# Optimization experiments

Hardware: AMD Instinct MI355X
Metric: run time of the kernel (lower is better)

Reference implementation:

```python
import jax, jax.numpy as jnp
import numpy as np
from jax import lax

B, C_IN, T = 64, 16, 8192
HID, OUT = 64, 10
NEW_T = T // 4            # two MaxPool1d(2)
N_NODES = B * NEW_T       # 131072
N_EDGES = 2_097_152       # avg degree 16


def setup_inputs() -> dict:
    key = jax.random.key(0)
    ks = jax.random.split(key, 8)
    x = jax.random.normal(ks[0], (B, C_IN, T), dtype=jnp.float32)
    edge_index = jax.random.randint(ks[1], (2, N_EDGES), 0, N_NODES, dtype=jnp.int32)
    s = 0.05
    return {
        "x": x,
        "edge_index": edge_index,
        "conv1_w": jax.random.normal(ks[2], (16, C_IN, 5), dtype=jnp.float32) * s,
        "conv1_b": jnp.zeros((16,), jnp.float32),
        "conv2_w": jax.random.normal(ks[3], (32, 16, 5), dtype=jnp.float32) * s,
        "conv2_b": jnp.zeros((32,), jnp.float32),
        "gcn1_w": jax.random.normal(ks[4], (32, HID), dtype=jnp.float32) * s,
        "gcn1_b": jnp.zeros((HID,), jnp.float32),
        "gcn2_w": jax.random.normal(ks[5], (HID, HID), dtype=jnp.float32) * s,
        "gcn2_b": jnp.zeros((HID,), jnp.float32),
        "cls_w": jax.random.normal(ks[6], (HID, OUT), dtype=jnp.float32) * s,
        "cls_b": jnp.zeros((OUT,), jnp.float32),
    }


def conv1d(x, w, b):
    # x: [B, Cin, T], w: [Cout, Cin, K], padding=2 -> same length
    y = lax.conv_general_dilated(x, w, window_strides=(1,), padding=[(2, 2)],
                                 dimension_numbers=("NCH", "OIH", "NCH"))
    return y + b[None, :, None]


def maxpool2(x):
    # non-overlapping MaxPool1d(kernel=2) over last dim
    b, c, t = x.shape
    return x.reshape(b, c, t // 2, 2).max(axis=-1)


def gcn_conv(x, edge_index, W, b, n):
    # PyG GCNConv: add self-loops, symmetric normalization, scatter-add aggregate
    row, col = edge_index[0], edge_index[1]   # source j, target i
    loop = jnp.arange(n, dtype=row.dtype)
    row = jnp.concatenate([row, loop])
    col = jnp.concatenate([col, loop])
    deg = jax.ops.segment_sum(jnp.ones(row.shape, x.dtype), col, num_segments=n)
    dis = jnp.where(deg > 0, lax.rsqrt(deg), jnp.zeros_like(deg))
    norm = dis[row] * dis[col]                # [E+N]
    xw = x @ W                                # [N, out]
    msg = xw[row] * norm[:, None]             # gather along edges
    out = jax.ops.segment_sum(msg, col, num_segments=n)
    return out + b


def reference(x, edge_index, conv1_w, conv1_b, conv2_w, conv2_b,
              gcn1_w, gcn1_b, gcn2_w, gcn2_b, cls_w, cls_b):
    h = maxpool2(jax.nn.relu(conv1d(x, conv1_w, conv1_b)))     # [B,16,T/2]
    h = maxpool2(jax.nn.relu(conv1d(h, conv2_w, conv2_b)))     # [B,32,T/4]
    feat = h.transpose(0, 2, 1).reshape(-1, 32)                # [B*new_T, 32]
    n = feat.shape[0]
    g = jax.nn.relu(gcn_conv(feat, edge_index, gcn1_w, gcn1_b, n))
    g = jax.nn.relu(gcn_conv(g, edge_index, gcn2_w, gcn2_b, n))
    pooled = g.reshape(B, -1, HID).mean(axis=1)                # [B, HID]
    return pooled @ cls_w + cls_b                               # [B, OUT]
```

## Files before the change

kernel.cpp:

```cpp
#include <hip/hip_runtime.h>
#include <hip/hip_bf16.h>
#include <hip/hip_fp16.h>

#define BATCH 64
#define C_IN 16
#define T0 8192
#define T1 4096
#define T2 2048
#define N_NODES (BATCH * T2)
#define HID 64
#define NOUT 10

#define NCB 256
#define CB_SHIFT 9
#define CB_TGT 512
#define RCAP 9216
#define PC_EDGES 2048
#define PC_CAP 28

#define PK_RMASK 0x1FFFF

#define EC 1024

#define ZROW N_NODES

#define ROWW 24

#define FP8_SCALE 256.0f
#define FP8_SINV  (1.0f / 256.0f)

typedef __fp16 half8 __attribute__((ext_vector_type(8)));
typedef __fp16 half4v __attribute__((ext_vector_type(4)));
typedef float floatx4 __attribute__((ext_vector_type(4)));
typedef float floatx2 __attribute__((ext_vector_type(2)));

__global__ __launch_bounds__(256) void conv1_kernel(const float* __restrict__ x,
    const float* __restrict__ w, const float* __restrict__ bias,
    __fp16* __restrict__ h1) {
  __shared__ __fp16 xs[528 * ROWW];
  int b = blockIdx.x >> 4;
  int tp0 = (blockIdx.x & 15) * 256;
  int t_base = 2 * tp0 - 8;
  const float* xb = x + (size_t)b * C_IN * T0;
  for (int idx = threadIdx.x; idx < 16 * 132; idx += 256) {
    int ci = idx & 15;
    int c4 = idx >> 4;
    int gt = t_base + c4 * 4;
    float4 v = make_float4(0.f, 0.f, 0.f, 0.f);
    if (gt >= 0 && gt + 4 <= T0) v = *(const float4*)(xb + ci * T0 + gt);
    __fp16* d = xs + (c4 * 4) * ROWW + ci;
    d[0] = (__fp16)v.x;
    d[ROWW] = (__fp16)v.y;
    d[2 * ROWW] = (__fp16)v.z;
    d[3 * ROWW] = (__fp16)v.w;
  }
  int ln = threadIdx.x & 15;
  int q = (threadIdx.x & 63) >> 4;
  int wib = threadIdx.x >> 6;
  half8 wb[3];
#pragma unroll
  for (int ks = 0; ks < 3; ++ks) {
    int kk = ks * 2 + (q >> 1);
#pragma unroll
    for (int j = 0; j < 8; ++j) {
      int ci = (q & 1) * 8 + j;
      float wv = (kk < 5) ? w[(ln * 16 + ci) * 5 + kk] : 0.f;
      wb[ks][j] = (__fp16)wv;
    }
  }
  float bv = bias[ln];
  __syncthreads();
  int qh = q >> 1, qo = (q & 1) * 8;
#pragma unroll 2
  for (int mtl = 0; mtl < 8; ++mtl) {
    int mt = wib * 8 + mtl;
    int posb = mt * 16 + ln + qh + 6;
    half8 a0 = *(const half8*)(xs + posb * ROWW + qo);
    half8 a1 = *(const half8*)(xs + (posb + 2) * ROWW + qo);
    half8 a2 = *(const half8*)(xs + (posb + 4) * ROWW + qo);
    floatx4 c0 = {0.f, 0.f, 0.f, 0.f};
    c0 = __builtin_amdgcn_mfma_f32_16x16x32_f16(a0, wb[0], c0, 0, 0, 0);
    c0 = __builtin_amdgcn_mfma_f32_16x16x32_f16(a1, wb[1], c0, 0, 0, 0);
    c0 = __builtin_amdgcn_mfma_f32_16x16x32_f16(a2, wb[2], c0, 0, 0, 0);
    int tp = tp0 + mt * 8 + q * 2;
    size_t o = ((size_t)b * T1 + tp) * 16 + ln;
    h1[o] = (__fp16)fmaxf(fmaxf(c0[0], c0[1]) + bv, 0.f);
    h1[o + 16] = (__fp16)fmaxf(fmaxf(c0[2], c0[3]) + bv, 0.f);
  }
}

__global__ __launch_bounds__(256) void conv2_gemm1(const __fp16* __restrict__ h1,
    const float* __restrict__ w, const float* __restrict__ bias,
    const float* __restrict__ W1, const float* __restrict__ dis,
    unsigned char* __restrict__ xw) {
  __shared__ __fp16 xs[520 * ROWW];
  __shared__ __fp16 fs[256 * 40];
  int b = blockIdx.x >> 3;
  int tp0 = (blockIdx.x & 7) * 256;
  int t_base = 2 * tp0 - 2;
  for (int idx = threadIdx.x; idx < 520 * 2; idx += 256) {
    int row = idx >> 1;
    int hf = idx & 1;
    int gt = t_base + row;
    half8 v;
#pragma unroll
    for (int j = 0; j < 8; ++j) v[j] = (__fp16)0.f;
    if (gt >= 0 && gt < T1) v = *(const half8*)(h1 + ((size_t)b * T1 + gt) * 16 + hf * 8);
    *(half8*)(xs + row * ROWW + hf * 8) = v;
  }
  int ln = threadIdx.x & 15;
  int q = (threadIdx.x & 63) >> 4;
  int wib = threadIdx.x >> 6;
  half8 wb[2][3];
#pragma unroll
  for (int nt = 0; nt < 2; ++nt)
#pragma unroll
    for (int ks = 0; ks < 3; ++ks) {
      int kk = ks * 2 + (q >> 1);
#pragma unroll
      for (int j = 0; j < 8; ++j) {
        int ci = (q & 1) * 8 + j;
        float wv = (kk < 5) ? w[((nt * 16 + ln) * 16 + ci) * 5 + kk] : 0.f;
        wb[nt][ks][j] = (__fp16)wv;
      }
    }
  float b20 = bias[ln];
  float b21 = bias[16 + ln];
  __syncthreads();
  int qh = q >> 1, qo = (q & 1) * 8;
#pragma unroll 2
  for (int mtl = 0; mtl < 8; ++mtl) {
    int mt = wib * 8 + mtl;
    int posb = mt * 16 + ln + qh;
    half8 a0 = *(const half8*)(xs + posb * ROWW + qo);
    half8 a1 = *(const half8*)(xs + (posb + 2) * ROWW + qo);
    half8 a2 = *(const half8*)(xs + (posb + 4) * ROWW + qo);
    floatx4 c0 = {0.f, 0.f, 0.f, 0.f};
    floatx4 c1 = {0.f, 0.f, 0.f, 0.f};
    c0 = __builtin_amdgcn_mfma_f32_16x16x32_f16(a0, wb[0][0], c0, 0, 0, 0);
    c0 = __builtin_amdgcn_mfma_f32_16x16x32_f16(a1, wb[0][1], c0, 0, 0, 0);
    c0 = __builtin_amdgcn_mfma_f32_16x16x32_f16(a2, wb[0][2], c0, 0, 0, 0);
    c1 = __builtin_amdgcn_mfma_f32_16x16x32_f16(a0, wb[1][0], c1, 0, 0, 0);
    c1 = __builtin_amdgcn_mfma_f32_16x16x32_f16(a1, wb[1][1], c1, 0, 0, 0);
    c1 = __builtin_amdgcn_mfma_f32_16x16x32_f16(a2, wb[1][2], c1, 0, 0, 0);
    int node = wib * 64 + mtl * 8 + q * 2;
    fs[node * 40 + ln] = (__fp16)fmaxf(fmaxf(c0[0], c0[1]) + b20, 0.f);
    fs[(node + 1) * 40 + ln] = (__fp16)fmaxf(fmaxf(c0[2], c0[3]) + b20, 0.f);
    fs[node * 40 + 16 + ln] = (__fp16)fmaxf(fmaxf(c1[0], c1[1]) + b21, 0.f);
    fs[(node + 1) * 40 + 16 + ln] = (__fp16)fmaxf(fmaxf(c1[2], c1[3]) + b21, 0.f);
  }
  half8 bf[4];
#pragma unroll
  for (int t = 0; t < 4; ++t)
#pragma unroll
    for (int j = 0; j < 8; ++j)
      bf[t][j] = (__fp16)W1[(q * 8 + j) * 64 + ln * 4 + t];
  int gnode0 = b * T2 + tp0;
#pragma unroll
  for (int tt = 0; tt < 4; ++tt) {
    int lbase = (wib * 4 + tt) * 16;
    half8 a = *(const half8*)(fs + (lbase + ln) * 40 + q * 8);
    float d[4];
#pragma unroll
    for (int r = 0; r < 4; ++r) d[r] = dis[gnode0 + lbase + q * 4 + r] * FP8_SCALE;
    floatx4 acc[4];
#pragma unroll
    for (int t = 0; t < 4; ++t) {
      floatx4 z = {0.f, 0.f, 0.f, 0.f};
      acc[t] = __builtin_amdgcn_mfma_f32_16x16x32_f16(a, bf[t], z, 0, 0, 0);
    }
#pragma unroll
    for (int r = 0; r < 4; ++r) {
      int u = __builtin_amdgcn_cvt_pk_fp8_f32(acc[0][r] * d[r], acc[1][r] * d[r], 0, 0);
      u = __builtin_amdgcn_cvt_pk_fp8_f32(acc[2][r] * d[r], acc[3][r] * d[r], u, 1);
      *(unsigned*)(xw + (size_t)(gnode0 + lbase + q * 4 + r) * 64 + ln * 4) = (unsigned)u;
    }
  }
}

__global__ __launch_bounds__(256) void partition_pairs(const int* __restrict__ ei, int E,
    int* __restrict__ rcnt, int* __restrict__ gpairs) {
  __shared__ int lcnt[NCB];
  __shared__ int lpk[NCB * PC_CAP];
  if (threadIdx.x < NCB) lcnt[threadIdx.x] = 0;
  __syncthreads();
  int e0 = blockIdx.x * PC_EDGES;
#pragma unroll
  for (int j = 0; j < PC_EDGES / 256; ++j) {
    int e = e0 + j * 256 + threadIdx.x;
    if (e < E) {
      int r = ei[e];
      int c = ei[E + e];
      int cb = c >> CB_SHIFT;
      int pk = r | ((c & (CB_TGT - 1)) << 17);
      int slot = atomicAdd(&lcnt[cb], 1);
      if (slot < PC_CAP) {
        lpk[cb * PC_CAP + slot] = pk;
      } else {
        int pos = atomicAdd(&rcnt[cb], 1);
        if (pos < RCAP) gpairs[(size_t)cb * RCAP + pos] = pk;
      }
    }
  }
  __syncthreads();
  int t = threadIdx.x;
  if (t < NCB) {
    int n = lcnt[t];
    if (n > PC_CAP) n = PC_CAP;
    if (n > 0) {
      int base = atomicAdd(&rcnt[t], n);
      int* dst = gpairs + (size_t)t * RCAP;
      for (int k = 0; k < n; ++k) {
        int p = base + k;
        if (p < RCAP) dst[p] = lpk[t * PC_CAP + k];
      }
    }
  }
}

__global__ __launch_bounds__(512) void build_csr(const int* __restrict__ gpairs,
    const int* __restrict__ rcnt, int* __restrict__ ebuf,
    int* __restrict__ estart, int* __restrict__ ecnt, float* __restrict__ dis) {
  __shared__ int deg[CB_TGT];
  __shared__ int cur[CB_TGT];
  __shared__ int sc[CB_TGT];
  __shared__ int wsum[8];
  int b = blockIdx.x;
  int t = threadIdx.x;
  deg[t] = 0;
  cur[t] = 0;
  __syncthreads();
  int m = rcnt[b];
  if (m > RCAP) m = RCAP;
  const int* reg = gpairs + (size_t)b * RCAP;
  for (int k = t; k < m; k += 512)
    atomicAdd(&deg[(reg[k] >> 17) & (CB_TGT - 1)], 1);
  __syncthreads();
  int d = deg[t];
  int lane = t & 63;
  int wv = t >> 6;
  int sum = d;
#pragma unroll
  for (int off = 1; off < 64; off <<= 1) {
    int v = __shfl_up(sum, off, 64);
    if (lane >= off) sum += v;
  }
  if (lane == 63) wsum[wv] = sum;
  __syncthreads();
  int prefix = 0;
#pragma unroll
  for (int i = 0; i < 8; ++i) prefix += (i < wv) ? wsum[i] : 0;
  int excl = prefix + sum - d;
  int gi = (b << CB_SHIFT) + t;
  int base = b * RCAP;
  estart[gi] = base + excl;
  ecnt[gi] = d;
  dis[gi] = rsqrtf((float)d + 1.0f);
  sc[t] = excl;
  __syncthreads();
  for (int k = t; k < m; k += 512) {
    int p = reg[k];
    int lc = (p >> 17) & (CB_TGT - 1);
    int off = atomicAdd(&cur[lc], 1);
    ebuf[base + sc[lc] + off] = p & PK_RMASK;
  }
}

#define GATHER_NODE(c_, stl_, ALO, AHI)                                         \
  {                                                                             \
    int sb_ = (stl_) + es;                                                      \
    int nf_ = (c_) >> 4;                                                        \
    for (int it = 0; it < nf_; ++it) {                                          \
      unsigned wv_[4];                                                          \
      _Pragma("unroll")                                                         \
      for (int j = 0; j < 4; ++j) {                                             \
        unsigned r = (unsigned)sidx[sb_ + (it << 4) + j * 4];                   \
        wv_[j] = *(const unsigned*)(tab + ((r << 6) + ch4));                    \
      }                                                                         \
      _Pragma("unroll")                                                         \
      for (int j = 0; j < 4; ++j) {                                             \
        ALO += __builtin_amdgcn_cvt_pk_f32_fp8(wv_[j], 0);                      \
        AHI += __builtin_amdgcn_cvt_pk_f32_fp8(wv_[j], 1);                      \
      }                                                                         \
    }                                                                           \
    if ((c_) & 15) {                                                            \
      int s0_ = nf_ << 4;                                                       \
      unsigned wv_[4];                                                          \
      _Pragma("unroll")                                                         \
      for (int j = 0; j < 4; ++j) {                                             \
        int k = s0_ + j * 4 + es;                                               \
        unsigned r = (unsigned)sidx[(stl_) + k];                                \
        unsigned off = (k < (c_)) ? ((r << 6) + ch4) : zoff;                    \
        wv_[j] = *(const unsigned*)(tab + off);                                 \
      }                                                                         \
      _Pragma("unroll")                                                         \
      for (int j = 0; j < 4; ++j) {                                             \
        ALO += __builtin_amdgcn_cvt_pk_f32_fp8(wv_[j], 0);                      \
        AHI += __builtin_amdgcn_cvt_pk_f32_fp8(wv_[j], 1);                      \
      }                                                                         \
    }                                                                           \
  }

__global__ __launch_bounds__(256) void agg1_gemm2(const unsigned char* __restrict__ tab,
    const int* __restrict__ ebuf, const int* __restrict__ estart,
    const int* __restrict__ ecnt, const float* __restrict__ dis,
    const float* __restrict__ bias, const float* __restrict__ W2,
    unsigned char* __restrict__ xw2, int N) {
  __shared__ __fp16 g1s[16 * 72];
  __shared__ int sidx[EC + 16];
  __shared__ int sst[16], scn[16];
  int t = threadIdx.x;
  int base16 = blockIdx.x * 16;
  if (t < 16) {
    sst[t] = estart[base16 + t];
    scn[t] = ecnt[base16 + t];
  }
  __syncthreads();
  int span0 = sst[0];
  int total = sst[15] + scn[15] - span0;
  if (total > EC) total = EC;
  for (int k = t; k < total; k += 256) sidx[k] = ebuf[span0 + k];
  __syncthreads();
  int lane = t & 63;
  int es = lane >> 4;
  int ch = lane & 15;
  int wib = t >> 6;
  unsigned ch4 = (unsigned)ch * 4u;
  unsigned zoff = ((unsigned)ZROW << 6) + ch4;
  float4 bv = *(const float4*)(bias + ch * 4);
#pragma unroll
  for (int jj = 0; jj < 4; ++jj) {
    int il = wib * 4 + jj;
    int i = base16 + il;
    int stl = sst[il] - span0;
    int c = scn[il];
    if (stl + c > EC) c = (EC > stl) ? (EC - stl) : 0;
    float di = dis[i] * FP8_SINV;
    floatx2 aLO = {0.f, 0.f}, aHI = {0.f, 0.f};
    GATHER_NODE(c, stl, aLO, aHI)
    float ax = aLO.x, ay = aLO.y, az = aHI.x, aw = aHI.y;
    ax += __shfl_xor(ax, 16, 64); ax += __shfl_xor(ax, 32, 64);
    ay += __shfl_xor(ay, 16, 64); ay += __shfl_xor(ay, 32, 64);
    az += __shfl_xor(az, 16, 64); az += __shfl_xor(az, 32, 64);
    aw += __shfl_xor(aw, 16, 64); aw += __shfl_xor(aw, 32, 64);
    unsigned sw = *(const unsigned*)(tab + (((unsigned)i << 6) + ch4));
    floatx2 slo = __builtin_amdgcn_cvt_pk_f32_fp8(sw, 0);
    floatx2 shi = __builtin_amdgcn_cvt_pk_f32_fp8(sw, 1);
    if (es == 0) {
      half4v r;
      r[0] = (__fp16)fmaxf((ax + slo.x) * di + bv.x, 0.f);
      r[1] = (__fp16)fmaxf((ay + slo.y) * di + bv.y, 0.f);
      r[2] = (__fp16)fmaxf((az + shi.x) * di + bv.z, 0.f);
      r[3] = (__fp16)fmaxf((aw + shi.y) * di + bv.w, 0.f);
      *(half4v*)(g1s + il * 72 + ch * 4) = r;
    }
  }
  __syncthreads();
  int m = lane & 15;
  int q = lane >> 4;
  half8 b0, b1;
#pragma unroll
  for (int j = 0; j < 8; ++j) {
    b0[j] = (__fp16)W2[(q * 8 + j) * 64 + wib * 16 + m];
    b1[j] = (__fp16)W2[(32 + q * 8 + j) * 64 + wib * 16 + m];
  }
  half8 a0 = *(const half8*)(g1s + m * 72 + q * 8);
  half8 a1 = *(const half8*)(g1s + m * 72 + 32 + q * 8);
  floatx4 acc = {0.f, 0.f, 0.f, 0.f};
  acc = __builtin_amdgcn_mfma_f32_16x16x32_f16(a0, b0, acc, 0, 0, 0);
  acc = __builtin_amdgcn_mfma_f32_16x16x32_f16(a1, b1, acc, 0, 0, 0);
  float sv[4];
#pragma unroll
  for (int r = 0; r < 4; ++r)
    sv[r] = acc[r] * dis[base16 + q * 4 + r] * FP8_SCALE;
  int u = __builtin_amdgcn_cvt_pk_fp8_f32(sv[0], sv[1], 0, 0);
  u = __builtin_amdgcn_cvt_pk_fp8_f32(sv[2], sv[3], u, 1);
#pragma unroll
  for (int r = 0; r < 4; ++r) {
    int node = base16 + q * 4 + r;
    xw2[(size_t)node * 64 + wib * 16 + m] = (unsigned char)(((unsigned)u) >> (8 * r));
  }
}

__global__ __launch_bounds__(256) void gcn_aggregate_pool(const unsigned char* __restrict__ tab,
    const int* __restrict__ ebuf, const int* __restrict__ estart,
    const int* __restrict__ ecnt, const float* __restrict__ dis,
    const float* __restrict__ bias, float* __restrict__ pool, int N) {
  __shared__ float4 red[4][16];
  __shared__ int sidx[EC + 16];
  __shared__ int sst[16], scn[16];
  int t = threadIdx.x;
  int base16 = blockIdx.x * 16;
  if (t < 16) {
    sst[t] = estart[base16 + t];
    scn[t] = ecnt[base16 + t];
  }
  __syncthreads();
  int span0 = sst[0];
  int total = sst[15] + scn[15] - span0;
  if (total > EC) total = EC;
  for (int k = t; k < total; k += 256) sidx[k] = ebuf[span0 + k];
  __syncthreads();
  int lane = t & 63;
  int es = lane >> 4;
  int ch = lane & 15;
  int wib = t >> 6;
  unsigned ch4 = (unsigned)ch * 4u;
  unsigned zoff = ((unsigned)ZROW << 6) + ch4;
  float4 bv = *(const float4*)(bias + ch * 4);
  float px = 0.f, py = 0.f, pz = 0.f, pw = 0.f;
#pragma unroll
  for (int jj = 0; jj < 4; ++jj) {
    int il = wib * 4 + jj;
    int i = base16 + il;
    int stl = sst[il] - span0;
    int c = scn[il];
    if (stl + c > EC) c = (EC > stl) ? (EC - stl) : 0;
    float di = dis[i] * FP8_SINV;
    floatx2 aLO = {0.f, 0.f}, aHI = {0.f, 0.f};
    GATHER_NODE(c, stl, aLO, aHI)
    float ax = aLO.x, ay = aLO.y, az = aHI.x, aw = aHI.y;
    ax += __shfl_xor(ax, 16, 64); ax += __shfl_xor(ax, 32, 64);
    ay += __shfl_xor(ay, 16, 64); ay += __shfl_xor(ay, 32, 64);
    az += __shfl_xor(az, 16, 64); az += __shfl_xor(az, 32, 64);
    aw += __shfl_xor(aw, 16, 64); aw += __shfl_xor(aw, 32, 64);
    unsigned sw = *(const unsigned*)(tab + (((unsigned)i << 6) + ch4));
    floatx2 slo = __builtin_amdgcn_cvt_pk_f32_fp8(sw, 0);
    floatx2 shi = __builtin_amdgcn_cvt_pk_f32_fp8(sw, 1);
    px += fmaxf((ax + slo.x) * di + bv.x, 0.f);
    py += fmaxf((ay + slo.y) * di + bv.y, 0.f);
    pz += fmaxf((az + shi.x) * di + bv.z, 0.f);
    pw += fmaxf((aw + shi.y) * di + bv.w, 0.f);
  }
  if (es == 0) red[wib][ch] = make_float4(px, py, pz, pw);
  __syncthreads();
  if (threadIdx.x < 64) {
    int f = threadIdx.x;
    int c4 = f >> 2, j4 = f & 3;
    const float* r0 = (const float*)&red[0][c4];
    const float* r1 = (const float*)&red[1][c4];
    const float* r2 = (const float*)&red[2][c4];
    const float* r3 = (const float*)&red[3][c4];
    float sum = r0[j4] + r1[j4] + r2[j4] + r3[j4];
    int b = (blockIdx.x * 16) >> 11;
    atomicAdd(&pool[b * 64 + f], sum);
  }
}

__global__ __launch_bounds__(64) void classify(const float* __restrict__ pool,
    const float* __restrict__ cw, const float* __restrict__ cb,
    float* __restrict__ out) {
  __shared__ float pl[64];
  int b = blockIdx.x;
  int t = threadIdx.x;
  pl[t] = pool[b * 64 + t] * (1.0f / (float)T2);
  __syncthreads();
  if (t < NOUT) {
    float a = cb[t];
#pragma unroll
    for (int k = 0; k < 64; ++k) a += pl[k] * cw[k * NOUT + t];
    out[b * NOUT + t] = a;
  }
}

extern "C" void kernel_launch(void* const* d_in, const int* in_sizes, int n_in,
                              void* d_out, int out_size, void* d_ws, size_t ws_size,
                              hipStream_t stream) {
  const float* x    = (const float*)d_in[0];
  const int*   ei   = (const int*)d_in[1];
  const float* c1w  = (const float*)d_in[2];
  const float* c1b  = (const float*)d_in[3];
  const float* c2w  = (const float*)d_in[4];
  const float* c2b  = (const float*)d_in[5];
  const float* g1w  = (const float*)d_in[6];
  const float* g1b  = (const float*)d_in[7];
  const float* g2w  = (const float*)d_in[8];
  const float* g2b  = (const float*)d_in[9];
  const float* cw   = (const float*)d_in[10];
  const float* cb   = (const float*)d_in[11];
  float* out = (float*)d_out;
  int E = in_sizes[1] / 2;
  const int N = N_NODES;

  char* ws = (char*)d_ws;
  int*    gpairs = (int*)(ws);
  int*    ebuf   = (int*)(ws + 9437184);
  int*    rcnt   = (int*)(ws + 18874368);
  int*    estart = (int*)(ws + 18878464);
  int*    ecnt   = (int*)(ws + 19402752);
  float*  dis    = (float*)(ws + 19927040);
  float*  pool   = (float*)(ws + 20451328);
  unsigned char* xw  = (unsigned char*)(ws + 20467712);
  unsigned char* xw2 = (unsigned char*)(ws + 37245184);
  __fp16* h1     = (__fp16*)(ws + 54022656);

  hipMemsetAsync(rcnt, 0, NCB * sizeof(int), stream);
  hipMemsetAsync(pool, 0, BATCH * HID * sizeof(float), stream);
  hipMemsetAsync(xw + (size_t)N * 64, 0, 64, stream);
  hipMemsetAsync(xw2 + (size_t)N * 64, 0, 64, stream);

  conv1_kernel<<<dim3(BATCH * 16), dim3(256), 0, stream>>>(x, c1w, c1b, h1);
  partition_pairs<<<dim3((E + PC_EDGES - 1) / PC_EDGES), dim3(256), 0, stream>>>(ei, E, rcnt, gpairs);
  build_csr<<<dim3(NCB), dim3(512), 0, stream>>>(gpairs, rcnt, ebuf, estart, ecnt, dis);

  conv2_gemm1<<<dim3(BATCH * 8), dim3(256), 0, stream>>>(h1, c2w, c2b, g1w, dis, xw);
  agg1_gemm2<<<dim3(N / 16), dim3(256), 0, stream>>>(xw, ebuf, estart, ecnt, dis, g1b, g2w, xw2, N);
  gcn_aggregate_pool<<<dim3(N / 16), dim3(256), 0, stream>>>(xw2, ebuf, estart, ecnt, dis, g2b, pool, N);

  classify<<<dim3(BATCH), dim3(64), 0, stream>>>(pool, cw, cb, out);
}
```

Baseline: 263.2 us.

## Software-pipeline edge gathers across nodes with double-buffered loads

The per-node gather loops in both aggregation kernels become one flattened loop over 16-edge windows spanning a wave's four nodes. Each window's loads are issued into one of two register buffers while the other buffer is consumed, so gather latency overlaps with the FP8 convert-and-accumulate. Self-loop rows and degree scales are loaded up front. This adds register pressure, branchier control flow and runtime selects in the per-node finalize step.

```diff
diff --git a/kernel.cpp b/kernel.cpp
--- a/kernel.cpp
+++ b/kernel.cpp
@@ -266,39 +266,75 @@
   }
 }
 
-#define GATHER_NODE(c_, stl_, ALO, AHI)                                         \
-  {                                                                             \
-    int sb_ = (stl_) + es;                                                      \
-    int nf_ = (c_) >> 4;                                                        \
-    for (int it = 0; it < nf_; ++it) {                                          \
-      unsigned wv_[4];                                                          \
-      _Pragma("unroll")                                                         \
-      for (int j = 0; j < 4; ++j) {                                             \
-        unsigned r = (unsigned)sidx[sb_ + (it << 4) + j * 4];                   \
-        wv_[j] = *(const unsigned*)(tab + ((r << 6) + ch4));                    \
-      }                                                                         \
-      _Pragma("unroll")                                                         \
-      for (int j = 0; j < 4; ++j) {                                             \
-        ALO += __builtin_amdgcn_cvt_pk_f32_fp8(wv_[j], 0);                      \
-        AHI += __builtin_amdgcn_cvt_pk_f32_fp8(wv_[j], 1);                      \
-      }                                                                         \
-    }                                                                           \
-    if ((c_) & 15) {                                                            \
-      int s0_ = nf_ << 4;                                                       \
-      unsigned wv_[4];                                                          \
-      _Pragma("unroll")                                                         \
-      for (int j = 0; j < 4; ++j) {                                             \
-        int k = s0_ + j * 4 + es;                                               \
-        unsigned r = (unsigned)sidx[(stl_) + k];                                \
-        unsigned off = (k < (c_)) ? ((r << 6) + ch4) : zoff;                    \
-        wv_[j] = *(const unsigned*)(tab + off);                                 \
-      }                                                                         \
-      _Pragma("unroll")                                                         \
-      for (int j = 0; j < 4; ++j) {                                             \
-        ALO += __builtin_amdgcn_cvt_pk_f32_fp8(wv_[j], 0);                      \
-        AHI += __builtin_amdgcn_cvt_pk_f32_fp8(wv_[j], 1);                      \
-      }                                                                         \
-    }                                                                           \
+#define ISSUEW(dst_, stl_, w_, c_)                                             \
+  if ((((w_) + 1) << 4) > (c_)) {                                              \
+    _Pragma("unroll")                                                          \
+    for (int j = 0; j < 4; ++j) {                                              \
+      int k = ((w_) << 4) + j * 4 + es;                                        \
+      unsigned r = (unsigned)sidx[(stl_) + k];                                 \
+      unsigned off = (k < (c_)) ? ((r << 6) + ch4) : zoff;                     \
+      dst_[j] = *(const unsigned*)(tab + off);                                 \
+    }                                                                          \
+  } else {                                                                     \
+    _Pragma("unroll")                                                          \
+    for (int j = 0; j < 4; ++j) {                                              \
+      unsigned r = (unsigned)sidx[(stl_) + ((w_) << 4) + j * 4 + es];          \
+      dst_[j] = *(const unsigned*)(tab + ((r << 6) + ch4));                    \
+    }                                                                          \
+  }
+#define CONSW(src_, ALO, AHI)                                                  \
+  _Pragma("unroll")                                                            \
+  for (int j = 0; j < 4; ++j) {                                                \
+    ALO += __builtin_amdgcn_cvt_pk_f32_fp8(src_[j], 0);                        \
+    AHI += __builtin_amdgcn_cvt_pk_f32_fp8(src_[j], 1);                        \
+  }
+#define GATHER_PIPE(FINALIZE_)                                                 \
+  {                                                                            \
+    int il0 = wib * 4;                                                         \
+    int totw = 0;                                                              \
+    _Pragma("unroll")                                                          \
+    for (int jj = 0; jj < 4; ++jj) {                                           \
+      int stlj = sst[il0 + jj] - span0;                                        \
+      int cj = scn[il0 + jj];                                                  \
+      if (stlj + cj > EC) cj = (EC > stlj) ? (EC - stlj) : 0;                  \
+      totw += cj ? ((cj + 15) >> 4) : 1;                                       \
+    }                                                                          \
+    int cil = il0;                                                             \
+    int cstl = sst[cil] - span0;                                               \
+    int cc = scn[cil];                                                         \
+    if (cstl + cc > EC) cc = (EC > cstl) ? (EC - cstl) : 0;                    \
+    int cnw = cc ? ((cc + 15) >> 4) : 1;                                       \
+    int cw = 0;                                                                \
+    unsigned wa_[4], wb_[4];                                                   \
+    ISSUEW(wa_, cstl, 0, cc)                                                   \
+    floatx2 aLO = {0.f, 0.f}, aHI = {0.f, 0.f};                                \
+    for (int s = 0; s < totw; ++s) {                                           \
+      int nil = cil, nw2 = cw + 1, nstl = cstl, nc = cc, nnw = cnw;            \
+      if (nw2 >= cnw) {                                                        \
+        nil = cil + 1;                                                         \
+        nw2 = 0;                                                               \
+        if (nil < il0 + 4) {                                                   \
+          nstl = sst[nil] - span0;                                             \
+          nc = scn[nil];                                                       \
+          if (nstl + nc > EC) nc = (EC > nstl) ? (EC - nstl) : 0;              \
+          nnw = nc ? ((nc + 15) >> 4) : 1;                                     \
+        }                                                                      \
+      }                                                                        \
+      int hav = (nil < il0 + 4);                                               \
+      if ((s & 1) == 0) {                                                      \
+        if (hav) { ISSUEW(wb_, nstl, nw2, nc) }                                \
+        CONSW(wa_, aLO, aHI)                                                   \
+      } else {                                                                 \
+        if (hav) { ISSUEW(wa_, nstl, nw2, nc) }                                \
+        CONSW(wb_, aLO, aHI)                                                   \
+      }                                                                        \
+      if (cw == cnw - 1) {                                                     \
+        FINALIZE_(cil)                                                         \
+        aLO = (floatx2)(0.f);                                                  \
+        aHI = (floatx2)(0.f);                                                  \
+      }                                                                        \
+      cil = nil; cw = nw2; cstl = nstl; cc = nc; cnw = nnw;                    \
+    }                                                                          \
   }
 
 __global__ __launch_bounds__(256) void agg1_gemm2(const unsigned char* __restrict__ tab,
@@ -328,33 +364,37 @@
   unsigned ch4 = (unsigned)ch * 4u;
   unsigned zoff = ((unsigned)ZROW << 6) + ch4;
   float4 bv = *(const float4*)(bias + ch * 4);
-#pragma unroll
-  for (int jj = 0; jj < 4; ++jj) {
-    int il = wib * 4 + jj;
-    int i = base16 + il;
-    int stl = sst[il] - span0;
-    int c = scn[il];
-    if (stl + c > EC) c = (EC > stl) ? (EC - stl) : 0;
-    float di = dis[i] * FP8_SINV;
-    floatx2 aLO = {0.f, 0.f}, aHI = {0.f, 0.f};
-    GATHER_NODE(c, stl, aLO, aHI)
-    float ax = aLO.x, ay = aLO.y, az = aHI.x, aw = aHI.y;
-    ax += __shfl_xor(ax, 16, 64); ax += __shfl_xor(ax, 32, 64);
-    ay += __shfl_xor(ay, 16, 64); ay += __shfl_xor(ay, 32, 64);
-    az += __shfl_xor(az, 16, 64); az += __shfl_xor(az, 32, 64);
-    aw += __shfl_xor(aw, 16, 64); aw += __shfl_xor(aw, 32, 64);
-    unsigned sw = *(const unsigned*)(tab + (((unsigned)i << 6) + ch4));
-    floatx2 slo = __builtin_amdgcn_cvt_pk_f32_fp8(sw, 0);
-    floatx2 shi = __builtin_amdgcn_cvt_pk_f32_fp8(sw, 1);
-    if (es == 0) {
-      half4v r;
-      r[0] = (__fp16)fmaxf((ax + slo.x) * di + bv.x, 0.f);
-      r[1] = (__fp16)fmaxf((ay + slo.y) * di + bv.y, 0.f);
-      r[2] = (__fp16)fmaxf((az + shi.x) * di + bv.z, 0.f);
-      r[3] = (__fp16)fmaxf((aw + shi.y) * di + bv.w, 0.f);
-      *(half4v*)(g1s + il * 72 + ch * 4) = r;
-    }
-  }
+  unsigned sw0 = *(const unsigned*)(tab + (((unsigned)(base16 + wib * 4 + 0) << 6) + ch4));
+  unsigned sw1 = *(const unsigned*)(tab + (((unsigned)(base16 + wib * 4 + 1) << 6) + ch4));
+  unsigned sw2 = *(const unsigned*)(tab + (((unsigned)(base16 + wib * 4 + 2) << 6) + ch4));
+  unsigned sw3 = *(const unsigned*)(tab + (((unsigned)(base16 + wib * 4 + 3) << 6) + ch4));
+  float d0 = dis[base16 + wib * 4 + 0] * FP8_SINV;
+  float d1 = dis[base16 + wib * 4 + 1] * FP8_SINV;
+  float d2 = dis[base16 + wib * 4 + 2] * FP8_SINV;
+  float d3 = dis[base16 + wib * 4 + 3] * FP8_SINV;
+#define FIN_AGG1(cil_)                                                         \
+  {                                                                            \
+    int jjc = (cil_) - wib * 4;                                                \
+    float di = (jjc == 0) ? d0 : (jjc == 1) ? d1 : (jjc == 2) ? d2 : d3;       \
+    unsigned sw = (jjc == 0) ? sw0 : (jjc == 1) ? sw1 : (jjc == 2) ? sw2 : sw3;\
+    float ax = aLO.x, ay = aLO.y, az = aHI.x, aw = aHI.y;                      \
+    ax += __shfl_xor(ax, 16, 64); ax += __shfl_xor(ax, 32, 64);                \
+    ay += __shfl_xor(ay, 16, 64); ay += __shfl_xor(ay, 32, 64);                \
+    az += __shfl_xor(az, 16, 64); az += __shfl_xor(az, 32, 64);                \
+    aw += __shfl_xor(aw, 16, 64); aw += __shfl_xor(aw, 32, 64);                \
+    floatx2 slo = __builtin_amdgcn_cvt_pk_f32_fp8(sw, 0);                      \
+    floatx2 shi = __builtin_amdgcn_cvt_pk_f32_fp8(sw, 1);                      \
+    if (es == 0) {                                                             \
+      half4v r;                                                                \
+      r[0] = (__fp16)fmaxf((ax + slo.x) * di + bv.x, 0.f);                     \
+      r[1] = (__fp16)fmaxf((ay + slo.y) * di + bv.y, 0.f);                     \
+      r[2] = (__fp16)fmaxf((az + shi.x) * di + bv.z, 0.f);                     \
+      r[3] = (__fp16)fmaxf((aw + shi.y) * di + bv.w, 0.f);                     \
+      *(half4v*)(g1s + (cil_) * 72 + ch * 4) = r;                              \
+    }                                                                          \
+  }
+  GATHER_PIPE(FIN_AGG1)
+#undef FIN_AGG1
   __syncthreads();
   int m = lane & 15;
   int q = lane >> 4;
@@ -408,30 +448,34 @@
   unsigned ch4 = (unsigned)ch * 4u;
   unsigned zoff = ((unsigned)ZROW << 6) + ch4;
   float4 bv = *(const float4*)(bias + ch * 4);
+  unsigned sw0 = *(const unsigned*)(tab + (((unsigned)(base16 + wib * 4 + 0) << 6) + ch4));
+  unsigned sw1 = *(const unsigned*)(tab + (((unsigned)(base16 + wib * 4 + 1) << 6) + ch4));
+  unsigned sw2 = *(const unsigned*)(tab + (((unsigned)(base16 + wib * 4 + 2) << 6) + ch4));
+  unsigned sw3 = *(const unsigned*)(tab + (((unsigned)(base16 + wib * 4 + 3) << 6) + ch4));
+  float d0 = dis[base16 + wib * 4 + 0] * FP8_SINV;
+  float d1 = dis[base16 + wib * 4 + 1] * FP8_SINV;
+  float d2 = dis[base16 + wib * 4 + 2] * FP8_SINV;
+  float d3 = dis[base16 + wib * 4 + 3] * FP8_SINV;
   float px = 0.f, py = 0.f, pz = 0.f, pw = 0.f;
-#pragma unroll
-  for (int jj = 0; jj < 4; ++jj) {
-    int il = wib * 4 + jj;
-    int i = base16 + il;
-    int stl = sst[il] - span0;
-    int c = scn[il];
-    if (stl + c > EC) c = (EC > stl) ? (EC - stl) : 0;
-    float di = dis[i] * FP8_SINV;
-    floatx2 aLO = {0.f, 0.f}, aHI = {0.f, 0.f};
-    GATHER_NODE(c, stl, aLO, aHI)
-    float ax = aLO.x, ay = aLO.y, az = aHI.x, aw = aHI.y;
-    ax += __shfl_xor(ax, 16, 64); ax += __shfl_xor(ax, 32, 64);
-    ay += __shfl_xor(ay, 16, 64); ay += __shfl_xor(ay, 32, 64);
-    az += __shfl_xor(az, 16, 64); az += __shfl_xor(az, 32, 64);
-    aw += __shfl_xor(aw, 16, 64); aw += __shfl_xor(aw, 32, 64);
-    unsigned sw = *(const unsigned*)(tab + (((unsigned)i << 6) + ch4));
-    floatx2 slo = __builtin_amdgcn_cvt_pk_f32_fp8(sw, 0);
-    floatx2 shi = __builtin_amdgcn_cvt_pk_f32_fp8(sw, 1);
-    px += fmaxf((ax + slo.x) * di + bv.x, 0.f);
-    py += fmaxf((ay + slo.y) * di + bv.y, 0.f);
-    pz += fmaxf((az + shi.x) * di + bv.z, 0.f);
-    pw += fmaxf((aw + shi.y) * di + bv.w, 0.f);
-  }
+#define FIN_POOL(cil_)                                                         \
+  {                                                                            \
+    int jjc = (cil_) - wib * 4;                                                \
+    float di = (jjc == 0) ? d0 : (jjc == 1) ? d1 : (jjc == 2) ? d2 : d3;       \
+    unsigned sw = (jjc == 0) ? sw0 : (jjc == 1) ? sw1 : (jjc == 2) ? sw2 : sw3;\
+    float ax = aLO.x, ay = aLO.y, az = aHI.x, aw = aHI.y;                      \
+    ax += __shfl_xor(ax, 16, 64); ax += __shfl_xor(ax, 32, 64);                \
+    ay += __shfl_xor(ay, 16, 64); ay += __shfl_xor(ay, 32, 64);                \
+    az += __shfl_xor(az, 16, 64); az += __shfl_xor(az, 32, 64);                \
+    aw += __shfl_xor(aw, 16, 64); aw += __shfl_xor(aw, 32, 64);                \
+    floatx2 slo = __builtin_amdgcn_cvt_pk_f32_fp8(sw, 0);                      \
+    floatx2 shi = __builtin_amdgcn_cvt_pk_f32_fp8(sw, 1);                      \
+    px += fmaxf((ax + slo.x) * di + bv.x, 0.f);                                \
+    py += fmaxf((ay + slo.y) * di + bv.y, 0.f);                                \
+    pz += fmaxf((az + shi.x) * di + bv.z, 0.f);                                \
+    pw += fmaxf((aw + shi.y) * di + bv.w, 0.f);                                \
+  }
+  GATHER_PIPE(FIN_POOL)
+#undef FIN_POOL
   if (es == 0) red[wib][ch] = make_float4(px, py, pz, pw);
   __syncthreads();
   if (threadIdx.x < 64) {
```

Result: slower. 269.4 us (+2.4%).
